# Kernel tuning notes

Measured on AMD Instinct MI355X. Metric: run time of the kernel, lower is better.

## Reference

```python
import jax, jax.numpy as jnp
import numpy as np


def setup_inputs() -> dict:
    key = jax.random.key(0)
    k1, k2, k3 = jax.random.split(key, 3)
    x = jax.random.normal(k1, (8, 3, 256, 256), dtype=jnp.float32)
    conv_w = jax.random.normal(k2, (64, 3), dtype=jnp.float32)  # 1x1 conv weight [O, C]
    w = jax.random.normal(k3, (64, 8), dtype=jnp.float32)       # per-channel LBP weights
    return {"x": x, "conv_w": conv_w, "w": w}


def _heaviside(d):
    # torch.heaviside(d, 0.): 1 where d > 0, else 0 (including d == 0)
    return jnp.where(d > 0, jnp.ones((), d.dtype), jnp.zeros((), d.dtype))


def reference(x, conv_w, w):
    # 1x1 conv, no bias: [N,C,H,W] x [O,C] -> [N,O,H,W]
    y = jnp.einsum('nchw,oc->nohw', x, conv_w)
    c = y[:, :, 1:-1, 1:-1]  # center, [N,O,H-2,W-2]
    # 8 neighbor shifts in the original order
    shifts = [
        y[:, :, 0:-2, 0:-2], y[:, :, 0:-2, 1:-1], y[:, :, 0:-2, 2:],
        y[:, :, 1:-1, 0:-2], y[:, :, 2:, 0:-2], y[:, :, 2:, 1:-1],
        y[:, :, 2:, 2:],    y[:, :, 1:-1, 2:],
    ]
    act = jnp.stack([_heaviside(c - s) for s in shifts], axis=2)  # [N,O,8,H-2,W-2]
    # weighted reduction over the 8 directions with exp(w)
    x_cat = jnp.einsum('nolhw,ol->nohw', act, jnp.exp(w))
    padded = jnp.pad(x_cat, ((0, 0), (0, 0), (1, 1), (1, 1)))  # ZeroPad2d(1)
    # res=True: concat raw input along channels -> [N, 3+O, H, W]
    return jnp.concatenate([x, padded], axis=1)
```

## Files before the change

kernel.cpp:

```cpp
#include <hip/hip_runtime.h>


__global__ __launch_bounds__(256) void lbp_all(
    const float* __restrict__ x,
    const float* __restrict__ conv_w,
    const float* __restrict__ w,
    float* __restrict__ out)
{
#pragma clang fp contract(off)
    const int n     = blockIdx.z;
    const int og    = blockIdx.y;
    const int tid   = threadIdx.x;
    const int lane  = tid & 63;
    const int wv    = tid >> 6;
    const int col   = lane * 4;
    const int hrow0 = blockIdx.x * 8 + wv * 2;

    __shared__ float ews[128];
    if (tid < 128) ews[tid] = expf(w[og * 128 + tid]);

    const float* xn = x + (size_t)n * 3 * 65536;

    float4 xr[4][3];
    #pragma unroll
    for (int r = 0; r < 4; ++r) {
        int row = hrow0 - 1 + r;
        row = row < 0 ? 0 : (row > 255 ? 255 : row);
        #pragma unroll
        for (int ch = 0; ch < 3; ++ch)
            xr[r][ch] = *(const float4*)(xn + (ch * 256 + row) * 256 + col);
    }

    if (og == 0) {
        #pragma unroll
        for (int ch = 0; ch < 3; ++ch) {
            float* cp = out + ((((size_t)n * 67 + ch) * 256 + hrow0) * 256 + col);
            *(float4*)cp         = xr[1][ch];
            *(float4*)(cp + 256) = xr[2][ch];
        }
    }

    __syncthreads();

    float* obase = out + ((((size_t)n * 67 + 3 + og * 16) * 256 + hrow0) * 256 + col);

    #pragma unroll 4
    for (int oi = 0; oi < 16; ++oi) {
        const int o = og * 16 + oi;
        const float cw0 = conv_w[o * 3 + 0];
        const float cw1 = conv_w[o * 3 + 1];
        const float cw2 = conv_w[o * 3 + 2];

        float Y[4][6];
        #pragma unroll
        for (int r = 0; r < 4; ++r) {
            float4 yv;
            yv.x = xr[r][0].x * cw0 + xr[r][1].x * cw1 + xr[r][2].x * cw2;
            yv.y = xr[r][0].y * cw0 + xr[r][1].y * cw1 + xr[r][2].y * cw2;
            yv.z = xr[r][0].z * cw0 + xr[r][1].z * cw1 + xr[r][2].z * cw2;
            yv.w = xr[r][0].w * cw0 + xr[r][1].w * cw1 + xr[r][2].w * cw2;
            Y[r][1] = yv.x; Y[r][2] = yv.y; Y[r][3] = yv.z; Y[r][4] = yv.w;
            Y[r][0] = __shfl_up(yv.w, 1);
            Y[r][5] = __shfl_down(yv.x, 1);
        }

        const float e0 = ews[oi * 8 + 0], e1 = ews[oi * 8 + 1];
        const float e2 = ews[oi * 8 + 2], e3 = ews[oi * 8 + 3];
        const float e4 = ews[oi * 8 + 4], e5 = ews[oi * 8 + 5];
        const float e6 = ews[oi * 8 + 6], e7 = ews[oi * 8 + 7];

        #pragma unroll
        for (int k = 0; k < 2; ++k) {
            const int hrow = hrow0 + k;
            float res[4];
            if (hrow == 0 || hrow == 255) {
                res[0] = res[1] = res[2] = res[3] = 0.f;
            } else {
                const float* up  = Y[k];
                const float* mid = Y[k + 1];
                const float* dn  = Y[k + 2];
                #pragma unroll
                for (int j = 0; j < 4; ++j) {
                    const float c = mid[j + 1];
                    float acc;
                    acc  = (c > up [j    ]) ? e0 : 0.f;
                    acc += (c > up [j + 1]) ? e1 : 0.f;
                    acc += (c > up [j + 2]) ? e2 : 0.f;
                    acc += (c > mid[j    ]) ? e3 : 0.f;
                    acc += (c > dn [j    ]) ? e4 : 0.f;
                    acc += (c > dn [j + 1]) ? e5 : 0.f;
                    acc += (c > dn [j + 2]) ? e6 : 0.f;
                    acc += (c > mid[j + 2]) ? e7 : 0.f;
                    res[j] = acc;
                }
                if (lane == 0)  res[0] = 0.f;
                if (lane == 63) res[3] = 0.f;
            }
            *(float4*)(obase + (size_t)oi * 65536 + (size_t)k * 256) =
                make_float4(res[0], res[1], res[2], res[3]);
        }
    }
}

extern "C" void kernel_launch(void* const* d_in, const int* in_sizes, int n_in,
                              void* d_out, int out_size, void* d_ws, size_t ws_size,
                              hipStream_t stream) {
    const float* x      = (const float*)d_in[0];
    const float* conv_w = (const float*)d_in[1];
    const float* w      = (const float*)d_in[2];
    float* out          = (float*)d_out;

    dim3 grid(32, 4, 8);
    dim3 block(256);
    hipLaunchKernelGGL(lbp_all, grid, block, 0, stream, x, conv_w, w, out);
}
```

Baseline: 152.5 us.

## Use nontemporal stores, scalarize LBP weights, and tune unroll and occupancy bounds

Output stores, including the raw input copy, become nontemporal vector stores so the write-only output does not pollute the caches. The exp weights are loaded as float4 from shared memory and moved into scalar registers with readfirstlane, which frees vector registers. The loop unroll drops from 4 to 2 and the launch bounds now request a minimum of 4 blocks per CU, trading instruction-level parallelism for occupancy. The kernel is store-bandwidth bound (about 140 MB of output), so the main lever is the store policy.

New measurement: 161.7 us. +6.0%, slower.

```diff
diff --git a/kernel.cpp b/kernel.cpp
--- a/kernel.cpp
+++ b/kernel.cpp
@@ -1,7 +1,18 @@
 #include <hip/hip_runtime.h>
 
 
-__global__ __launch_bounds__(256) void lbp_all(
+typedef float vfloat4 __attribute__((ext_vector_type(4)));
+
+__device__ __forceinline__ void store_nt4(float* p, float a, float b, float c, float d) {
+    vfloat4 v; v.x = a; v.y = b; v.z = c; v.w = d;
+    __builtin_nontemporal_store(v, (vfloat4*)p);
+}
+
+__device__ __forceinline__ void store_nt4f(float* p, float4 v) {
+    store_nt4(p, v.x, v.y, v.z, v.w);
+}
+
+__global__ __launch_bounds__(256, 4) void lbp_all(
     const float* __restrict__ x,
     const float* __restrict__ conv_w,
     const float* __restrict__ w,
@@ -35,8 +46,8 @@
         #pragma unroll
         for (int ch = 0; ch < 3; ++ch) {
             float* cp = out + ((((size_t)n * 67 + ch) * 256 + hrow0) * 256 + col);
-            *(float4*)cp         = xr[1][ch];
-            *(float4*)(cp + 256) = xr[2][ch];
+            store_nt4f(cp,       xr[1][ch]);
+            store_nt4f(cp + 256, xr[2][ch]);
         }
     }
 
@@ -44,8 +55,19 @@
 
     float* obase = out + ((((size_t)n * 67 + 3 + og * 16) * 256 + hrow0) * 256 + col);
 
-    #pragma unroll 4
+    #pragma unroll 2
     for (int oi = 0; oi < 16; ++oi) {
+        const float4 eA = *(const float4*)&ews[oi * 8 + 0];
+        const float4 eB = *(const float4*)&ews[oi * 8 + 4];
+        const float e0 = __uint_as_float(__builtin_amdgcn_readfirstlane(__float_as_uint(eA.x)));
+        const float e1 = __uint_as_float(__builtin_amdgcn_readfirstlane(__float_as_uint(eA.y)));
+        const float e2 = __uint_as_float(__builtin_amdgcn_readfirstlane(__float_as_uint(eA.z)));
+        const float e3 = __uint_as_float(__builtin_amdgcn_readfirstlane(__float_as_uint(eA.w)));
+        const float e4 = __uint_as_float(__builtin_amdgcn_readfirstlane(__float_as_uint(eB.x)));
+        const float e5 = __uint_as_float(__builtin_amdgcn_readfirstlane(__float_as_uint(eB.y)));
+        const float e6 = __uint_as_float(__builtin_amdgcn_readfirstlane(__float_as_uint(eB.z)));
+        const float e7 = __uint_as_float(__builtin_amdgcn_readfirstlane(__float_as_uint(eB.w)));
+
         const int o = og * 16 + oi;
         const float cw0 = conv_w[o * 3 + 0];
         const float cw1 = conv_w[o * 3 + 1];
@@ -63,11 +85,6 @@
             Y[r][0] = __shfl_up(yv.w, 1);
             Y[r][5] = __shfl_down(yv.x, 1);
         }
-
-        const float e0 = ews[oi * 8 + 0], e1 = ews[oi * 8 + 1];
-        const float e2 = ews[oi * 8 + 2], e3 = ews[oi * 8 + 3];
-        const float e4 = ews[oi * 8 + 4], e5 = ews[oi * 8 + 5];
-        const float e6 = ews[oi * 8 + 6], e7 = ews[oi * 8 + 7];
 
         #pragma unroll
         for (int k = 0; k < 2; ++k) {
@@ -96,8 +113,8 @@
                 if (lane == 0)  res[0] = 0.f;
                 if (lane == 63) res[3] = 0.f;
             }
-            *(float4*)(obase + (size_t)oi * 65536 + (size_t)k * 256) =
-                make_float4(res[0], res[1], res[2], res[3]);
+            store_nt4(obase + (size_t)oi * 65536 + (size_t)k * 256,
+                      res[0], res[1], res[2], res[3]);
         }
     }
 }
```
